# Performance work log

Measured on AMD Instinct MI355X. Metric: run time of the kernel, lower is better.

## Reference

```python
import jax, jax.numpy as jnp
import numpy as np

B = 1024          # global batch
D = 512           # embedding_size
C = 100000        # num_classes (sum over 8 shards)
S = 64.0          # ArcFace scale
M = 0.5           # ArcFace additive angular margin
EPS = 1e-30


def setup_inputs() -> dict:
    key = jax.random.key(0)
    k1, k2, k3 = jax.random.split(key, 3)
    embeddings = jax.random.normal(k1, (B, D), dtype=jnp.float32)
    weight = jax.random.normal(k2, (C, D), dtype=jnp.float32)
    labels = jax.random.randint(k3, (B,), 0, C, dtype=jnp.int64)
    return {"embeddings": embeddings, "weight": weight, "labels": labels}


def reference(embeddings, weight, labels):
    # normalize(embeddings), normalize(weight) -> cosine logits
    ne = embeddings * jax.lax.rsqrt(jnp.sum(embeddings * embeddings, axis=1, keepdims=True))
    nw = weight * jax.lax.rsqrt(jnp.sum(weight * weight, axis=1, keepdims=True))
    logits = jnp.clip(jnp.einsum("bd,cd->bc", ne, nw), -1.0, 1.0)  # [B, C]

    rows = jnp.arange(B)
    target_logit = logits[rows, labels]
    # ArcFace: cos(theta + m), theta+m clipped to pi (insightface CombinedMarginLoss m2)
    theta = jnp.arccos(jnp.clip(target_logit, -1.0, 1.0))
    new_target = jnp.cos(jnp.minimum(theta + M, jnp.float32(np.pi)))
    logits = logits.at[rows, labels].set(new_target) * S

    # FusedDistCrossEntropy (single-device equivalent): stable softmax,
    # gather target prob, loss = -mean(log(clamp(p_target, 1e-30)))
    logp = jax.nn.log_softmax(logits, axis=1)
    p_target = jnp.exp(logp[rows, labels])
    loss = -jnp.mean(jnp.log(jnp.maximum(p_target, EPS)))
    return loss
```

## Files before the change

### kernel.cpp

```cpp
#include <hip/hip_runtime.h>
#include <hip/hip_bf16.h>
#include <math.h>
#include <stdint.h>

#define B_BATCH   1024
#define D_DIM     512
#define C_CLASSES 100000
#define BM        128
#define BN        128
#define BK        32
#define KITERS    (D_DIM / BK)
#define MTILES    (B_BATCH / BM)
#define NTILES    ((C_CLASSES + BN - 1) / BN)
#define NGROUPS   98
#define GRID_G    (8 * 8 * NGROUPS)
#define LOG2E     1.44269504088896340736f
#define COSM      0.87758256189037276f
#define SINM      0.47942553860420301f
#define NEG_LOG_EPS 69.07755278982137f

typedef short bf16x8 __attribute__((ext_vector_type(8)));
typedef float f32x4  __attribute__((ext_vector_type(4)));

static __device__ __forceinline__ unsigned short f2bf(float f) {
    unsigned int u = __builtin_bit_cast(unsigned int, f);
    u += 0x7fffu + ((u >> 16) & 1u);
    return (unsigned short)(u >> 16);
}

static __device__ __forceinline__ unsigned int pk_bf16_trunc(float lo, float hi) {
    return __builtin_amdgcn_perm(__builtin_bit_cast(unsigned int, hi),
                                 __builtin_bit_cast(unsigned int, lo),
                                 0x07060302u);
}

static __device__ __forceinline__ void gld16(const unsigned short* g, unsigned short* l) {
    __builtin_amdgcn_global_load_lds(
        (const __attribute__((address_space(1))) unsigned int*)g,
        (__attribute__((address_space(3))) unsigned int*)l, 16, 0, 0);
}

__global__ __launch_bounds__(256) void norm_embed(const float* __restrict__ E,
                                                  unsigned short* __restrict__ Abf) {
    const int b = blockIdx.x;
    const int t = threadIdx.x;
    float2 v = ((const float2*)(E + (size_t)b * D_DIM))[t];
    float ss = v.x * v.x + v.y * v.y;
    #pragma unroll
    for (int off = 1; off < 64; off <<= 1) ss += __shfl_xor(ss, off);
    __shared__ float ws4[4];
    if ((t & 63) == 0) ws4[t >> 6] = ss;
    __syncthreads();
    float inv = rsqrtf(ws4[0] + ws4[1] + ws4[2] + ws4[3]);
    unsigned int packed = (unsigned int)f2bf(v.x * inv) |
                          ((unsigned int)f2bf(v.y * inv) << 16);
    ((unsigned int*)Abf)[(size_t)b * (D_DIM / 2) + t] = packed;
}

__global__ __launch_bounds__(256) void norm_weight(const float* __restrict__ W,
                                                   unsigned short* __restrict__ Wbf) {
    const int wave = threadIdx.x >> 6;
    const int lane = threadIdx.x & 63;
    const int row0 = blockIdx.x * 8 + wave * 2;
    const int row1 = row0 + 1;
    const float4* s0 = (const float4*)(W + (size_t)row0 * D_DIM);
    const float4* s1 = (const float4*)(W + (size_t)row1 * D_DIM);
    float4 a0 = s0[lane];
    float4 a1 = s0[lane + 64];
    float4 b0 = s1[lane];
    float4 b1 = s1[lane + 64];
    float sa = a0.x*a0.x + a0.y*a0.y + a0.z*a0.z + a0.w*a0.w
             + a1.x*a1.x + a1.y*a1.y + a1.z*a1.z + a1.w*a1.w;
    float sb = b0.x*b0.x + b0.y*b0.y + b0.z*b0.z + b0.w*b0.w
             + b1.x*b1.x + b1.y*b1.y + b1.z*b1.z + b1.w*b1.w;
    #pragma unroll
    for (int off = 1; off < 64; off <<= 1) {
        sa += __shfl_xor(sa, off);
        sb += __shfl_xor(sb, off);
    }
    float ia = rsqrtf(sa), ib = rsqrtf(sb);
    uint2* d0 = (uint2*)(Wbf + (size_t)row0 * D_DIM);
    uint2* d1 = (uint2*)(Wbf + (size_t)row1 * D_DIM);
    uint2 oa0 = {pk_bf16_trunc(a0.x*ia, a0.y*ia), pk_bf16_trunc(a0.z*ia, a0.w*ia)};
    uint2 oa1 = {pk_bf16_trunc(a1.x*ia, a1.y*ia), pk_bf16_trunc(a1.z*ia, a1.w*ia)};
    uint2 ob0 = {pk_bf16_trunc(b0.x*ib, b0.y*ib), pk_bf16_trunc(b0.z*ib, b0.w*ib)};
    uint2 ob1 = {pk_bf16_trunc(b1.x*ib, b1.y*ib), pk_bf16_trunc(b1.z*ib, b1.w*ib)};
    d0[lane] = oa0; d0[lane + 64] = oa1;
    d1[lane] = ob0; d1[lane + 64] = ob1;
}

static __device__ __forceinline__ float epi_term(float accv, int col, int lab,
                                                 float* __restrict__ st, int srow) {
    float c = fminf(1.f, fmaxf(-1.f, accv));
    if (col >= C_CLASSES) return 0.f;
    float s = c * 64.0f;
    if (col == lab) {
        float sn = sqrtf(fmaxf(0.f, 1.f - c * c));
        float nm = c * COSM - sn * SINM;
        if (c < -COSM) nm = -1.f;
        s = nm * 64.0f;
        st[srow] = s;
    }
    return exp2f((s - 64.0f) * LOG2E);
}

__global__ __launch_bounds__(256, 4) void gemm_cos(const unsigned short* __restrict__ Abf,
                                                   const unsigned short* __restrict__ Wbf,
                                                   const int* __restrict__ labels,
                                                   float* __restrict__ st,
                                                   float* __restrict__ partial) {
    __shared__ unsigned short As[BM * BK];
    __shared__ unsigned short Bs[BN * BK];
    __shared__ float rowSum[BM];
    __shared__ int   labs[BM];

    const int id = blockIdx.x;
    const int x  = id & 7;
    const int s  = id >> 3;
    const int mt = s & 7;
    const int y  = x + 8 * (s >> 3);
    if (y >= NTILES) return;
    const int m0 = mt * BM;
    const int n0 = y * BN;

    const int tid = threadIdx.x;
    if (tid < BM) { labs[tid] = labels[m0 + tid]; rowSum[tid] = 0.f; }

    const int lane = tid & 63;
    const int wave = tid >> 6;
    const int wm = wave & 1, wn = wave >> 1;
    const int l15 = lane & 15, quad = lane >> 4;

    const int rsub = lane >> 2;
    const int cg   = (lane & 3) * 8;
    const int c0 = wave * 2, c1 = wave * 2 + 1;
    const unsigned short* gA0 = Abf + (size_t)(m0 + c0 * 16 + rsub) * D_DIM + cg;
    const unsigned short* gA1 = Abf + (size_t)(m0 + c1 * 16 + rsub) * D_DIM + cg;
    const int bR0 = min(n0 + c0 * 16 + rsub, C_CLASSES - 1);
    const int bR1 = min(n0 + c1 * 16 + rsub, C_CLASSES - 1);
    const unsigned short* gB0 = Wbf + (size_t)bR0 * D_DIM + cg;
    const unsigned short* gB1 = Wbf + (size_t)bR1 * D_DIM + cg;
    unsigned short* lA0 = &As[c0 * 512];
    unsigned short* lA1 = &As[c1 * 512];
    unsigned short* lB0 = &Bs[c0 * 512];
    unsigned short* lB1 = &Bs[c1 * 512];

    const f32x4 z = (f32x4){0.f, 0.f, 0.f, 0.f};
    f32x4 a00 = z, a01 = z, a02 = z, a03 = z;
    f32x4 a10 = z, a11 = z, a12 = z, a13 = z;
    f32x4 a20 = z, a21 = z, a22 = z, a23 = z;
    f32x4 a30 = z, a31 = z, a32 = z, a33 = z;

    const int aro = (wm * 64 + l15) * BK + quad * 8;
    const int bro = (wn * 64 + l15) * BK + quad * 8;

    for (int kk = 0; kk < KITERS; ++kk) {
        __syncthreads();
        gld16(gA0, lA0); gld16(gA1, lA1);
        gld16(gB0, lB0); gld16(gB1, lB1);
        gA0 += BK; gA1 += BK; gB0 += BK; gB1 += BK;
        __syncthreads();

        bf16x8 af0 = *(const bf16x8*)&As[aro];
        bf16x8 af1 = *(const bf16x8*)&As[aro + 16 * BK];
        bf16x8 af2 = *(const bf16x8*)&As[aro + 32 * BK];
        bf16x8 af3 = *(const bf16x8*)&As[aro + 48 * BK];
        bf16x8 bf0 = *(const bf16x8*)&Bs[bro];
        bf16x8 bf1 = *(const bf16x8*)&Bs[bro + 16 * BK];
        bf16x8 bf2 = *(const bf16x8*)&Bs[bro + 32 * BK];
        bf16x8 bf3 = *(const bf16x8*)&Bs[bro + 48 * BK];

        a00 = __builtin_amdgcn_mfma_f32_16x16x32_bf16(af0, bf0, a00, 0, 0, 0);
        a01 = __builtin_amdgcn_mfma_f32_16x16x32_bf16(af0, bf1, a01, 0, 0, 0);
        a02 = __builtin_amdgcn_mfma_f32_16x16x32_bf16(af0, bf2, a02, 0, 0, 0);
        a03 = __builtin_amdgcn_mfma_f32_16x16x32_bf16(af0, bf3, a03, 0, 0, 0);
        a10 = __builtin_amdgcn_mfma_f32_16x16x32_bf16(af1, bf0, a10, 0, 0, 0);
        a11 = __builtin_amdgcn_mfma_f32_16x16x32_bf16(af1, bf1, a11, 0, 0, 0);
        a12 = __builtin_amdgcn_mfma_f32_16x16x32_bf16(af1, bf2, a12, 0, 0, 0);
        a13 = __builtin_amdgcn_mfma_f32_16x16x32_bf16(af1, bf3, a13, 0, 0, 0);
        a20 = __builtin_amdgcn_mfma_f32_16x16x32_bf16(af2, bf0, a20, 0, 0, 0);
        a21 = __builtin_amdgcn_mfma_f32_16x16x32_bf16(af2, bf1, a21, 0, 0, 0);
        a22 = __builtin_amdgcn_mfma_f32_16x16x32_bf16(af2, bf2, a22, 0, 0, 0);
        a23 = __builtin_amdgcn_mfma_f32_16x16x32_bf16(af2, bf3, a23, 0, 0, 0);
        a30 = __builtin_amdgcn_mfma_f32_16x16x32_bf16(af3, bf0, a30, 0, 0, 0);
        a31 = __builtin_amdgcn_mfma_f32_16x16x32_bf16(af3, bf1, a31, 0, 0, 0);
        a32 = __builtin_amdgcn_mfma_f32_16x16x32_bf16(af3, bf2, a32, 0, 0, 0);
        a33 = __builtin_amdgcn_mfma_f32_16x16x32_bf16(af3, bf3, a33, 0, 0, 0);
    }

    const int colbase = n0 + wn * 64 + l15;

    #define EPIROW(A0, A1, A2, A3, MI)                                         \
    {                                                                          \
        _Pragma("unroll")                                                      \
        for (int r = 0; r < 4; ++r) {                                          \
            const int rloc = wm * 64 + (MI) * 16 + quad * 4 + r;               \
            const int lab = labs[rloc];                                        \
            float part = 0.f;                                                  \
            part += epi_term((A0)[r], colbase,      lab, st, m0 + rloc);       \
            part += epi_term((A1)[r], colbase + 16, lab, st, m0 + rloc);       \
            part += epi_term((A2)[r], colbase + 32, lab, st, m0 + rloc);       \
            part += epi_term((A3)[r], colbase + 48, lab, st, m0 + rloc);       \
            part += __shfl_xor(part, 1);                                       \
            part += __shfl_xor(part, 2);                                       \
            part += __shfl_xor(part, 4);                                       \
            part += __shfl_xor(part, 8);                                       \
            if (l15 == 0) atomicAdd(&rowSum[rloc], part);                      \
        }                                                                      \
    }

    EPIROW(a00, a01, a02, a03, 0)
    EPIROW(a10, a11, a12, a13, 1)
    EPIROW(a20, a21, a22, a23, 2)
    EPIROW(a30, a31, a32, a33, 3)
    #undef EPIROW

    __syncthreads();
    if (tid < BM) partial[(size_t)(m0 + tid) * NTILES + y] = rowSum[tid];
}

__global__ __launch_bounds__(64) void reduce_loss(const float* __restrict__ partial,
                                                  const float* __restrict__ st,
                                                  float* __restrict__ out) {
    const int b = blockIdx.x;
    const int l = threadIdx.x;
    const float* row = partial + (size_t)b * NTILES;
    float L = 0.f;
    for (int t = l; t < NTILES; t += 64) L += row[t];
    #pragma unroll
    for (int off = 1; off < 64; off <<= 1) L += __shfl_xor(L, off);
    if (l == 0) {
        float logp = st[b] - 64.0f - logf(L);
        float lossb = fminf(-logp, NEG_LOG_EPS) * (1.0f / (float)B_BATCH);
        atomicAdd(out, lossb);
    }
}

extern "C" void kernel_launch(void* const* d_in, const int* in_sizes, int n_in,
                              void* d_out, int out_size, void* d_ws, size_t ws_size,
                              hipStream_t stream) {
    const float* emb = (const float*)d_in[0];
    const float* wgt = (const float*)d_in[1];
    const int*   lab = (const int*)d_in[2];
    float* out = (float*)d_out;
    char* ws = (char*)d_ws;

    const size_t WBF_B = (size_t)C_CLASSES * D_DIM * 2;
    const size_t ABF_B = (size_t)B_BATCH * D_DIM * 2;

    unsigned short* Wbf = (unsigned short*)ws;
    unsigned short* Abf = (unsigned short*)(ws + WBF_B);
    float* st      = (float*)(ws + WBF_B + ABF_B);
    float* partial = (float*)(ws + WBF_B + ABF_B + 4096);

    hipMemsetAsync(d_out, 0, sizeof(float), stream);
    norm_embed<<<B_BATCH, 256, 0, stream>>>(emb, Abf);
    norm_weight<<<C_CLASSES / 8, 256, 0, stream>>>(wgt, Wbf);
    gemm_cos<<<GRID_G, 256, 0, stream>>>(Abf, Wbf, lab, st, partial);
    reduce_loss<<<B_BATCH, 64, 0, stream>>>(partial, st, out);
}
```

Measured before the change: 457.8 us.

## Rewrite GEMM as 256x256 double-buffered tiles with swizzled LDS and XCD remap

Replaces the 128x128x32 single-buffered GEMM with 256x256x64 tiles in 512-thread blocks, double-buffered LDS loaded via global_load_lds. Loads are interleaved with MFMA phases under setprio, LDS rows are XOR-swizzled to avoid bank conflicts, and block IDs are remapped so contiguous tiles land on the same XCD. The goal is more data reuse per tile and loads hidden behind compute. The cost is heavy register use (128 accumulator floats per thread) and fewer blocks in flight.

```diff
diff --git a/kernel.cpp b/kernel.cpp
--- a/kernel.cpp
+++ b/kernel.cpp
@@ -6,14 +6,13 @@
 #define B_BATCH   1024
 #define D_DIM     512
 #define C_CLASSES 100000
-#define BM        128
-#define BN        128
-#define BK        32
-#define KITERS    (D_DIM / BK)
-#define MTILES    (B_BATCH / BM)
-#define NTILES    ((C_CLASSES + BN - 1) / BN)
-#define NGROUPS   98
-#define GRID_G    (8 * 8 * NGROUPS)
+#define BM        256
+#define BN        256
+#define BK        64
+#define KT        (D_DIM / BK)
+#define MT4       (B_BATCH / BM)
+#define NT256     ((C_CLASSES + BN - 1) / BN)
+#define GRID_G    (MT4 * NT256)
 #define LOG2E     1.44269504088896340736f
 #define COSM      0.87758256189037276f
 #define SINM      0.47942553860420301f
@@ -21,6 +20,10 @@
 
 typedef short bf16x8 __attribute__((ext_vector_type(8)));
 typedef float f32x4  __attribute__((ext_vector_type(4)));
+
+#define FENCE asm volatile("" ::: "memory")
+#define BAR() do { FENCE; __builtin_amdgcn_s_barrier(); FENCE; } while (0)
+#define VMW0() asm volatile("s_waitcnt vmcnt(0)" ::: "memory")
 
 static __device__ __forceinline__ unsigned short f2bf(float f) {
     unsigned int u = __builtin_bit_cast(unsigned int, f);
@@ -104,119 +107,193 @@
     return exp2f((s - 64.0f) * LOG2E);
 }
 
-__global__ __launch_bounds__(256, 4) void gemm_cos(const unsigned short* __restrict__ Abf,
+__global__ __launch_bounds__(512, 2) void gemm_cos(const unsigned short* __restrict__ Abf,
                                                    const unsigned short* __restrict__ Wbf,
                                                    const int* __restrict__ labels,
                                                    float* __restrict__ st,
                                                    float* __restrict__ partial) {
-    __shared__ unsigned short As[BM * BK];
-    __shared__ unsigned short Bs[BN * BK];
+    __shared__ __align__(16) unsigned short sA[2 * 256 * 64];
+    __shared__ __align__(16) unsigned short sB[2 * 256 * 64];
     __shared__ float rowSum[BM];
     __shared__ int   labs[BM];
 
-    const int id = blockIdx.x;
-    const int x  = id & 7;
-    const int s  = id >> 3;
-    const int mt = s & 7;
-    const int y  = x + 8 * (s >> 3);
-    if (y >= NTILES) return;
+    const int orig = blockIdx.x;
+    const int xcd  = orig & 7;
+    const int pos  = orig >> 3;
+    const int qq   = GRID_G >> 3;
+    const int rr   = GRID_G & 7;
+    const int wg   = (xcd < rr ? xcd * (qq + 1) : rr * (qq + 1) + (xcd - rr) * qq) + pos;
+    const int mt = wg & 3;
+    const int nt = wg >> 2;
     const int m0 = mt * BM;
-    const int n0 = y * BN;
-
-    const int tid = threadIdx.x;
-    if (tid < BM) { labs[tid] = labels[m0 + tid]; rowSum[tid] = 0.f; }
-
+    const int n0 = nt * BN;
+
+    const int tid  = threadIdx.x;
     const int lane = tid & 63;
     const int wave = tid >> 6;
-    const int wm = wave & 1, wn = wave >> 1;
+    const int wm = wave & 1;
+    const int wn = wave >> 1;
     const int l15 = lane & 15, quad = lane >> 4;
 
-    const int rsub = lane >> 2;
-    const int cg   = (lane & 3) * 8;
-    const int c0 = wave * 2, c1 = wave * 2 + 1;
-    const unsigned short* gA0 = Abf + (size_t)(m0 + c0 * 16 + rsub) * D_DIM + cg;
-    const unsigned short* gA1 = Abf + (size_t)(m0 + c1 * 16 + rsub) * D_DIM + cg;
-    const int bR0 = min(n0 + c0 * 16 + rsub, C_CLASSES - 1);
-    const int bR1 = min(n0 + c1 * 16 + rsub, C_CLASSES - 1);
-    const unsigned short* gB0 = Wbf + (size_t)bR0 * D_DIM + cg;
-    const unsigned short* gB1 = Wbf + (size_t)bR1 * D_DIM + cg;
-    unsigned short* lA0 = &As[c0 * 512];
-    unsigned short* lA1 = &As[c1 * 512];
-    unsigned short* lB0 = &Bs[c0 * 512];
-    unsigned short* lB1 = &Bs[c1 * 512];
+    if (tid < BM) { labs[tid] = labels[m0 + tid]; rowSum[tid] = 0.f; }
+
+    const int srow  = wave * 8 + (lane >> 3);
+    const int scolb = (((lane & 7) ^ (lane >> 3)) << 4);
+    const char* gA[2][2];
+    const char* gB[2][2];
+    #pragma unroll
+    for (int h = 0; h < 2; ++h)
+        #pragma unroll
+        for (int i = 0; i < 2; ++i) {
+            gA[h][i] = (const char*)Abf + (size_t)(m0 + h * 128 + i * 64 + srow) * (D_DIM * 2) + scolb;
+            int rB = min(n0 + h * 128 + i * 64 + srow, C_CLASSES - 1);
+            gB[h][i] = (const char*)Wbf + (size_t)rB * (D_DIM * 2) + scolb;
+        }
+
+    {
+        unsigned short* dA = sA + wave * 512;
+        unsigned short* dB = sB + wave * 512;
+        #pragma unroll
+        for (int h = 0; h < 2; ++h)
+            #pragma unroll
+            for (int i = 0; i < 2; ++i) {
+                gld16((const unsigned short*)gA[h][i], dA + h * 8192 + i * 4096);
+                gA[h][i] += 128;
+                gld16((const unsigned short*)gB[h][i], dB + h * 8192 + i * 4096);
+                gB[h][i] += 128;
+            }
+    }
 
     const f32x4 z = (f32x4){0.f, 0.f, 0.f, 0.f};
-    f32x4 a00 = z, a01 = z, a02 = z, a03 = z;
-    f32x4 a10 = z, a11 = z, a12 = z, a13 = z;
-    f32x4 a20 = z, a21 = z, a22 = z, a23 = z;
-    f32x4 a30 = z, a31 = z, a32 = z, a33 = z;
-
-    const int aro = (wm * 64 + l15) * BK + quad * 8;
-    const int bro = (wn * 64 + l15) * BK + quad * 8;
-
-    for (int kk = 0; kk < KITERS; ++kk) {
-        __syncthreads();
-        gld16(gA0, lA0); gld16(gA1, lA1);
-        gld16(gB0, lB0); gld16(gB1, lB1);
-        gA0 += BK; gA1 += BK; gB0 += BK; gB1 += BK;
-        __syncthreads();
-
-        bf16x8 af0 = *(const bf16x8*)&As[aro];
-        bf16x8 af1 = *(const bf16x8*)&As[aro + 16 * BK];
-        bf16x8 af2 = *(const bf16x8*)&As[aro + 32 * BK];
-        bf16x8 af3 = *(const bf16x8*)&As[aro + 48 * BK];
-        bf16x8 bf0 = *(const bf16x8*)&Bs[bro];
-        bf16x8 bf1 = *(const bf16x8*)&Bs[bro + 16 * BK];
-        bf16x8 bf2 = *(const bf16x8*)&Bs[bro + 32 * BK];
-        bf16x8 bf3 = *(const bf16x8*)&Bs[bro + 48 * BK];
-
-        a00 = __builtin_amdgcn_mfma_f32_16x16x32_bf16(af0, bf0, a00, 0, 0, 0);
-        a01 = __builtin_amdgcn_mfma_f32_16x16x32_bf16(af0, bf1, a01, 0, 0, 0);
-        a02 = __builtin_amdgcn_mfma_f32_16x16x32_bf16(af0, bf2, a02, 0, 0, 0);
-        a03 = __builtin_amdgcn_mfma_f32_16x16x32_bf16(af0, bf3, a03, 0, 0, 0);
-        a10 = __builtin_amdgcn_mfma_f32_16x16x32_bf16(af1, bf0, a10, 0, 0, 0);
-        a11 = __builtin_amdgcn_mfma_f32_16x16x32_bf16(af1, bf1, a11, 0, 0, 0);
-        a12 = __builtin_amdgcn_mfma_f32_16x16x32_bf16(af1, bf2, a12, 0, 0, 0);
-        a13 = __builtin_amdgcn_mfma_f32_16x16x32_bf16(af1, bf3, a13, 0, 0, 0);
-        a20 = __builtin_amdgcn_mfma_f32_16x16x32_bf16(af2, bf0, a20, 0, 0, 0);
-        a21 = __builtin_amdgcn_mfma_f32_16x16x32_bf16(af2, bf1, a21, 0, 0, 0);
-        a22 = __builtin_amdgcn_mfma_f32_16x16x32_bf16(af2, bf2, a22, 0, 0, 0);
-        a23 = __builtin_amdgcn_mfma_f32_16x16x32_bf16(af2, bf3, a23, 0, 0, 0);
-        a30 = __builtin_amdgcn_mfma_f32_16x16x32_bf16(af3, bf0, a30, 0, 0, 0);
-        a31 = __builtin_amdgcn_mfma_f32_16x16x32_bf16(af3, bf1, a31, 0, 0, 0);
-        a32 = __builtin_amdgcn_mfma_f32_16x16x32_bf16(af3, bf2, a32, 0, 0, 0);
-        a33 = __builtin_amdgcn_mfma_f32_16x16x32_bf16(af3, bf3, a33, 0, 0, 0);
+    f32x4 acc[8][4];
+    #pragma unroll
+    for (int m = 0; m < 8; ++m)
+        #pragma unroll
+        for (int n = 0; n < 4; ++n) acc[m][n] = z;
+
+    bf16x8 af[4][2];
+    bf16x8 bfr[4][2];
+
+    const int qsw = ((quad ^ (l15 & 7)) << 4);
+
+    for (int t = 0; t < KT; ++t) {
+        const int p  = t & 1;
+        const int pn = p ^ 1;
+
+        VMW0();
+        BAR();
+
+        const char* pa = (const char*)sA + (size_t)p * 32768 + (size_t)(wm * 128 + l15) * 128;
+        const char* pb = (const char*)sB + (size_t)p * 32768 + (size_t)(wn * 64  + l15) * 128;
+
+        #pragma unroll
+        for (int m = 0; m < 4; ++m)
+            #pragma unroll
+            for (int kh = 0; kh < 2; ++kh)
+                af[m][kh] = *(const bf16x8*)(pa + m * 2048 + (qsw ^ (kh << 6)));
+        #pragma unroll
+        for (int n = 0; n < 2; ++n)
+            #pragma unroll
+            for (int kh = 0; kh < 2; ++kh)
+                bfr[n][kh] = *(const bf16x8*)(pb + n * 2048 + (qsw ^ (kh << 6)));
+        if (t < KT - 1) {
+            unsigned short* dA = sA + pn * 16384 + wave * 512;
+            #pragma unroll
+            for (int h = 0; h < 2; ++h)
+                #pragma unroll
+                for (int i = 0; i < 2; ++i) {
+                    gld16((const unsigned short*)gA[h][i], dA + h * 8192 + i * 4096);
+                    gA[h][i] += 128;
+                }
+        }
+        BAR();
+        __builtin_amdgcn_s_setprio(1);
+        #pragma unroll
+        for (int m = 0; m < 4; ++m)
+            #pragma unroll
+            for (int n = 0; n < 2; ++n)
+                #pragma unroll
+                for (int kh = 0; kh < 2; ++kh)
+                    acc[m][n] = __builtin_amdgcn_mfma_f32_16x16x32_bf16(af[m][kh], bfr[n][kh], acc[m][n], 0, 0, 0);
+        __builtin_amdgcn_s_setprio(0);
+        BAR();
+
+        #pragma unroll
+        for (int n = 2; n < 4; ++n)
+            #pragma unroll
+            for (int kh = 0; kh < 2; ++kh)
+                bfr[n][kh] = *(const bf16x8*)(pb + n * 2048 + (qsw ^ (kh << 6)));
+        if (t < KT - 1) {
+            unsigned short* dB = sB + pn * 16384 + wave * 512;
+            #pragma unroll
+            for (int h = 0; h < 2; ++h)
+                #pragma unroll
+                for (int i = 0; i < 2; ++i) {
+                    gld16((const unsigned short*)gB[h][i], dB + h * 8192 + i * 4096);
+                    gB[h][i] += 128;
+                }
+        }
+        BAR();
+        __builtin_amdgcn_s_setprio(1);
+        #pragma unroll
+        for (int m = 0; m < 4; ++m)
+            #pragma unroll
+            for (int n = 2; n < 4; ++n)
+                #pragma unroll
+                for (int kh = 0; kh < 2; ++kh)
+                    acc[m][n] = __builtin_amdgcn_mfma_f32_16x16x32_bf16(af[m][kh], bfr[n][kh], acc[m][n], 0, 0, 0);
+        __builtin_amdgcn_s_setprio(0);
+        BAR();
+
+        #pragma unroll
+        for (int m = 0; m < 4; ++m)
+            #pragma unroll
+            for (int kh = 0; kh < 2; ++kh)
+                af[m][kh] = *(const bf16x8*)(pa + 8192 + m * 2048 + (qsw ^ (kh << 6)));
+        BAR();
+        __builtin_amdgcn_s_setprio(1);
+        #pragma unroll
+        for (int m = 0; m < 4; ++m)
+            #pragma unroll
+            for (int n = 2; n < 4; ++n)
+                #pragma unroll
+                for (int kh = 0; kh < 2; ++kh)
+                    acc[4 + m][n] = __builtin_amdgcn_mfma_f32_16x16x32_bf16(af[m][kh], bfr[n][kh], acc[4 + m][n], 0, 0, 0);
+        __builtin_amdgcn_s_setprio(0);
+        BAR();
+
+        __builtin_amdgcn_s_setprio(1);
+        #pragma unroll
+        for (int m = 0; m < 4; ++m)
+            #pragma unroll
+            for (int n = 0; n < 2; ++n)
+                #pragma unroll
+                for (int kh = 0; kh < 2; ++kh)
+                    acc[4 + m][n] = __builtin_amdgcn_mfma_f32_16x16x32_bf16(af[m][kh], bfr[n][kh], acc[4 + m][n], 0, 0, 0);
+        __builtin_amdgcn_s_setprio(0);
     }
 
     const int colbase = n0 + wn * 64 + l15;
-
-    #define EPIROW(A0, A1, A2, A3, MI)                                         \
-    {                                                                          \
-        _Pragma("unroll")                                                      \
-        for (int r = 0; r < 4; ++r) {                                          \
-            const int rloc = wm * 64 + (MI) * 16 + quad * 4 + r;               \
-            const int lab = labs[rloc];                                        \
-            float part = 0.f;                                                  \
-            part += epi_term((A0)[r], colbase,      lab, st, m0 + rloc);       \
-            part += epi_term((A1)[r], colbase + 16, lab, st, m0 + rloc);       \
-            part += epi_term((A2)[r], colbase + 32, lab, st, m0 + rloc);       \
-            part += epi_term((A3)[r], colbase + 48, lab, st, m0 + rloc);       \
-            part += __shfl_xor(part, 1);                                       \
-            part += __shfl_xor(part, 2);                                       \
-            part += __shfl_xor(part, 4);                                       \
-            part += __shfl_xor(part, 8);                                       \
-            if (l15 == 0) atomicAdd(&rowSum[rloc], part);                      \
-        }                                                                      \
-    }
-
-    EPIROW(a00, a01, a02, a03, 0)
-    EPIROW(a10, a11, a12, a13, 1)
-    EPIROW(a20, a21, a22, a23, 2)
-    EPIROW(a30, a31, a32, a33, 3)
-    #undef EPIROW
+    #pragma unroll
+    for (int m = 0; m < 8; ++m) {
+        #pragma unroll
+        for (int r = 0; r < 4; ++r) {
+            const int rloc = wm * 128 + m * 16 + quad * 4 + r;
+            const int lab = labs[rloc];
+            float part = 0.f;
+            #pragma unroll
+            for (int n = 0; n < 4; ++n)
+                part += epi_term(acc[m][n][r], colbase + n * 16, lab, st, m0 + rloc);
+            part += __shfl_xor(part, 1);
+            part += __shfl_xor(part, 2);
+            part += __shfl_xor(part, 4);
+            part += __shfl_xor(part, 8);
+            if (l15 == 0) atomicAdd(&rowSum[rloc], part);
+        }
+    }
 
     __syncthreads();
-    if (tid < BM) partial[(size_t)(m0 + tid) * NTILES + y] = rowSum[tid];
+    if (tid < BM) partial[(size_t)(m0 + tid) * NT256 + nt] = rowSum[tid];
 }
 
 __global__ __launch_bounds__(64) void reduce_loss(const float* __restrict__ partial,
@@ -224,9 +301,9 @@
                                                   float* __restrict__ out) {
     const int b = blockIdx.x;
     const int l = threadIdx.x;
-    const float* row = partial + (size_t)b * NTILES;
+    const float* row = partial + (size_t)b * NT256;
     float L = 0.f;
-    for (int t = l; t < NTILES; t += 64) L += row[t];
+    for (int t = l; t < NT256; t += 64) L += row[t];
     #pragma unroll
     for (int off = 1; off < 64; off <<= 1) L += __shfl_xor(L, off);
     if (l == 0) {
@@ -256,6 +333,6 @@
     hipMemsetAsync(d_out, 0, sizeof(float), stream);
     norm_embed<<<B_BATCH, 256, 0, stream>>>(emb, Abf);
     norm_weight<<<C_CLASSES / 8, 256, 0, stream>>>(wgt, Wbf);
-    gemm_cos<<<GRID_G, 256, 0, stream>>>(Abf, Wbf, lab, st, partial);
+    gemm_cos<<<GRID_G, 512, 0, stream>>>(Abf, Wbf, lab, st, partial);
     reduce_loss<<<B_BATCH, 64, 0, stream>>>(partial, st, out);
 }
```

New measurement: 512.4 us. +11.9%, slower.
